# Kernel tuning notes

Hardware: AMD Instinct MI355X
Metric: run time of the kernel (lower is better)

## Reference

```python
import jax, jax.numpy as jnp
import numpy as np

EMSIZE = 1024
NHEAD = 16
HEAD = EMSIZE // NHEAD


def setup_inputs() -> dict:
    key = jax.random.key(0)
    ks = jax.random.split(key, 8)
    s = 1.0 / np.sqrt(EMSIZE)
    return {
        "embed": jax.random.normal(ks[0], (2, 2048, EMSIZE), dtype=jnp.float32),
        "q": jax.random.normal(ks[1], (2, 2048, EMSIZE), dtype=jnp.float32),
        "Wk": jax.random.normal(ks[2], (EMSIZE, EMSIZE), dtype=jnp.float32) * s,
        "bk": jnp.zeros((EMSIZE,), dtype=jnp.float32),
        "Wq": jax.random.normal(ks[3], (EMSIZE, EMSIZE), dtype=jnp.float32) * s,
        "bq": jnp.zeros((EMSIZE,), dtype=jnp.float32),
        "Wv": jax.random.normal(ks[4], (EMSIZE, EMSIZE), dtype=jnp.float32) * s,
        "bv": jnp.zeros((EMSIZE,), dtype=jnp.float32),
    }


def _split_heads(x):
    # [b, s, E] -> [b, h, s, d]
    b, s, _ = x.shape
    return x.reshape(b, s, NHEAD, HEAD).transpose(0, 2, 1, 3)


def reference(embed, q, Wk, bk, Wq, bq, Wv, bv):
    # torch Linear: y = x @ W.T + b
    k = _split_heads(embed @ Wk.T + bk)   # [b, h, skv, d]
    qh = _split_heads(q @ Wq.T + bq)      # [b, h, sq, d]
    v = _split_heads(embed @ Wv.T + bv)   # [b, h, skv, d]
    scale = 1.0 / np.sqrt(HEAD).astype(np.float32)
    scores = jnp.einsum("bhqd,bhkd->bhqk", qh, k) * scale
    attn = jax.nn.softmax(scores, axis=-1)  # dropout p=0 -> identity
    ctx = jnp.einsum("bhqk,bhkd->bhqd", attn, v)
    b, h, sq, d = ctx.shape
    return ctx.transpose(0, 2, 1, 3).reshape(b, sq, h * d)
```

## Files before the change

kernel.cpp:

```cpp
#include <hip/hip_runtime.h>
#include <cstdint>
#include <cstddef>


using bf16 = __bf16;
typedef __bf16 bf16x8 __attribute__((ext_vector_type(8)));
typedef float f32x4 __attribute__((ext_vector_type(4)));
typedef float f32x16 __attribute__((ext_vector_type(16)));
using uint32 = unsigned int;

__device__ __forceinline__ void async16(void* lds, const void* g) {
  __builtin_amdgcn_global_load_lds((__attribute__((address_space(1))) void*)g,
                                   (__attribute__((address_space(3))) void*)lds,
                                   16, 0, 0);
}

__device__ __forceinline__ uint32 pack_bf16x2(float lo, float hi_) {
  union { bf16 h[2]; uint32 u; } w;
  w.h[0] = (bf16)lo; w.h[1] = (bf16)hi_;
  return w.u;
}

__global__ void cast_all_kernel(const float* __restrict__ e, const float* __restrict__ q,
                                const float* __restrict__ wk, const float* __restrict__ wq,
                                const float* __restrict__ wv, bf16* __restrict__ dst) {
  int i = blockIdx.x * blockDim.x + threadIdx.x;
  if (i >= 2883584) return;
  const float* src; int off;
  if (i < 1048576)      { src = e;  off = 0; }
  else if (i < 2097152) { src = q;  off = 1048576; }
  else if (i < 2359296) { src = wk; off = 2097152; }
  else if (i < 2621440) { src = wq; off = 2359296; }
  else                  { src = wv; off = 2621440; }
  float4 v = reinterpret_cast<const float4*>(src)[i - off];
  union { bf16 h[4]; unsigned long long u; } o;
  o.h[0] = (bf16)v.x; o.h[1] = (bf16)v.y; o.h[2] = (bf16)v.z; o.h[3] = (bf16)v.w;
  reinterpret_cast<unsigned long long*>(dst)[i] = o.u;
}

__global__ __launch_bounds__(256) void proj_kernel(
    const bf16* __restrict__ emb, const bf16* __restrict__ qin,
    const bf16* __restrict__ wk, const bf16* __restrict__ wq, const bf16* __restrict__ wv,
    const float* __restrict__ bk, const float* __restrict__ bq, const float* __restrict__ bv,
    bf16* __restrict__ Kp, bf16* __restrict__ Qp, bf16* __restrict__ Vt)
{
  __shared__ bf16 As[128 * 64];
  __shared__ bf16 Bs[128 * 64];

  int pid = blockIdx.x;
  int proj = pid >> 8;
  int t = pid & 255;
  int m0 = (t >> 3) * 128;
  int n0 = (t & 7) * 128;

  const bf16* A = (proj == 1) ? qin : emb;
  const bf16* W = (proj == 0) ? wk : (proj == 1) ? wq : wv;
  const float* bias = (proj == 0) ? bk : (proj == 1) ? bq : bv;
  const bool proj2 = (proj == 2);

  int tid = threadIdx.x;
  int lane = tid & 63, wid = tid >> 6;
  int quad = lane >> 4, l16 = lane & 15;
  int moff = (wid & 1) * 64, noff = (wid >> 1) * 64;

  f32x4 zero = {0.f, 0.f, 0.f, 0.f};
  f32x4 acc[4][4];
#pragma unroll
  for (int i = 0; i < 4; i++)
#pragma unroll
    for (int j = 0; j < 4; j++) acc[i][j] = zero;

  for (int kk = 0; kk < 1024; kk += 64) {
    __syncthreads();
#pragma unroll
    for (int i = 0; i < 4; i++) {
      int c = i * 256 + tid;
      int row = c >> 3;
      int ko = ((c ^ row) & 7) << 3;
      async16(&As[(size_t)(i * 256 + wid * 64) * 8], &A[(size_t)(m0 + row) * 1024 + kk + ko]);
      async16(&Bs[(size_t)(i * 256 + wid * 64) * 8], &W[(size_t)(n0 + row) * 1024 + kk + ko]);
    }
    __syncthreads();
#pragma unroll
    for (int ks = 0; ks < 2; ks++) {
      bf16x8 af[4], bfr[4];
#pragma unroll
      for (int i = 0; i < 4; i++) {
        int row = moff + i * 16 + l16;
        af[i] = *reinterpret_cast<const bf16x8*>(&As[row * 64 + ((((ks << 2) | quad) ^ row) & 7) * 8]);
      }
#pragma unroll
      for (int j = 0; j < 4; j++) {
        int row = noff + j * 16 + l16;
        bfr[j] = *reinterpret_cast<const bf16x8*>(&Bs[row * 64 + ((((ks << 2) | quad) ^ row) & 7) * 8]);
      }
      if (proj2) {
#pragma unroll
        for (int i = 0; i < 4; i++)
#pragma unroll
          for (int j = 0; j < 4; j++)
            acc[i][j] = __builtin_amdgcn_mfma_f32_16x16x32_bf16(bfr[j], af[i], acc[i][j], 0, 0, 0);
      } else {
#pragma unroll
        for (int i = 0; i < 4; i++)
#pragma unroll
          for (int j = 0; j < 4; j++)
            acc[i][j] = __builtin_amdgcn_mfma_f32_16x16x32_bf16(af[i], bfr[j], acc[i][j], 0, 0, 0);
      }
    }
  }

  if (proj2) {
#pragma unroll
    for (int i = 0; i < 4; i++) {
      int grow = m0 + moff + i * 16 + l16;
      int bb = grow >> 11;
      int ss = grow & 2047;
#pragma unroll
      for (int j = 0; j < 4; j++) {
#pragma unroll
        for (int r = 0; r < 4; r++) {
          int gcol = n0 + noff + j * 16 + quad * 4 + r;
          int hh = gcol >> 6, dd = gcol & 63;
          int bh = bb * 16 + hh;
          float v = acc[i][j][r] + bias[gcol];
          Vt[((size_t)bh * 64 + dd) * 2048 + ss] = (bf16)v;
        }
      }
    }
  } else {
    float bvv[4];
#pragma unroll
    for (int j = 0; j < 4; j++) bvv[j] = bias[n0 + noff + j * 16 + l16];
    bf16* dst = (proj == 0) ? Kp : Qp;
    const float qs = (proj == 1) ? 0.18033688011112042f : 1.0f;
#pragma unroll
    for (int i = 0; i < 4; i++) {
#pragma unroll
      for (int r = 0; r < 4; r++) {
        int grow = m0 + moff + i * 16 + quad * 4 + r;
        int bb = grow >> 11;
        int ss = grow & 2047;
#pragma unroll
        for (int j = 0; j < 4; j++) {
          int gcol = n0 + noff + j * 16 + l16;
          int hh = gcol >> 6, dd = gcol & 63;
          int bh = bb * 16 + hh;
          float v = (acc[i][j][r] + bvv[j]) * qs;
          dst[((size_t)bh * 2048 + ss) * 64 + dd] = (bf16)v;
        }
      }
    }
  }
}

__global__ __launch_bounds__(256, 2) void attn_kernel(
    const bf16* __restrict__ Qp, const bf16* __restrict__ Kp, const bf16* __restrict__ Vt,
    float* __restrict__ out)
{
  __shared__ bf16 Ks[2][64 * 64];
  __shared__ bf16 Vs[2][64 * 64];

  int swz = (blockIdx.x & 7) * 64 + (blockIdx.x >> 3);
  int qblk = swz & 15;
  int bh = swz >> 4;
  int q0 = qblk << 7;
  int bb = bh >> 4, hh = bh & 15;

  const bf16* Qg = Qp + (size_t)bh * (2048 * 64);
  const bf16* Kg = Kp + (size_t)bh * (2048 * 64);
  const bf16* Vg = Vt + (size_t)bh * (64 * 2048);

  int tid = threadIdx.x, lane = tid & 63, wid = tid >> 6;
  int l32 = lane & 31;
  int h = lane >> 5;
  int wq0 = q0 + wid * 32;

  auto stage = [&](int kt_, int buf) {
#pragma unroll
    for (int i = 0; i < 2; i++) {
      int c = i * 256 + tid;
      int row = c >> 3;
      int srow = (row & ~12) | ((row & 4) << 1) | ((row & 8) >> 1);
      int ko = ((c ^ row) & 7) << 3;
      async16(&Ks[buf][(size_t)(i * 256 + wid * 64) * 8], &Kg[(size_t)(kt_ * 64 + srow) * 64 + ko]);
      async16(&Vs[buf][(size_t)(i * 256 + wid * 64) * 8], &Vg[(size_t)row * 2048 + kt_ * 64 + ko]);
    }
  };

  bf16x8 qf[4];
#pragma unroll
  for (int s = 0; s < 4; s++)
    qf[s] = *reinterpret_cast<const bf16x8*>(
        &Qg[(size_t)(wq0 + l32) * 64 + s * 16 + h * 8]);

  stage(0, 0);

  const f32x16 z16 = {0.f, 0.f, 0.f, 0.f, 0.f, 0.f, 0.f, 0.f,
                      0.f, 0.f, 0.f, 0.f, 0.f, 0.f, 0.f, 0.f};
  f32x16 Ov[2];
  Ov[0] = z16; Ov[1] = z16;
  float2 l2;
  l2.x = 0.f; l2.y = 0.f;

  for (int kt = 0; kt < 32; kt++) {
    int cur = kt & 1;
    __syncthreads();
    __builtin_amdgcn_sched_barrier(0);
    if (kt < 31) stage(kt + 1, cur ^ 1);
    __builtin_amdgcn_sched_barrier(0);

    const bf16* Kc = Ks[cur];
    const bf16* Vc = Vs[cur];

#pragma unroll
    for (int t = 0; t < 2; t++) {
      f32x16 St;
      int row = t * 32 + l32;
      {
        bf16x8 kf = *reinterpret_cast<const bf16x8*>(&Kc[row * 64 + ((h ^ row) & 7) * 8]);
        St = __builtin_amdgcn_mfma_f32_32x32x16_bf16(kf, qf[0], z16, 0, 0, 0);
      }
#pragma unroll
      for (int s = 1; s < 4; s++) {
        int j8 = s * 2 + h;
        bf16x8 kf = *reinterpret_cast<const bf16x8*>(&Kc[row * 64 + ((j8 ^ row) & 7) * 8]);
        St = __builtin_amdgcn_mfma_f32_32x32x16_bf16(kf, qf[s], St, 0, 0, 0);
      }

      uint32 pk[8];
#pragma unroll
      for (int i = 0; i < 8; i++) {
        float pe = __builtin_amdgcn_exp2f(St[2 * i]);
        float po = __builtin_amdgcn_exp2f(St[2 * i + 1]);
        l2.x += pe; l2.y += po;
        pk[i] = pack_bf16x2(pe, po);
      }

#pragma unroll
      for (int g = 0; g < 2; g++) {
        union { uint32 u[4]; bf16x8 v; } pb;
#pragma unroll
        for (int i = 0; i < 4; i++) pb.u[i] = pk[g * 4 + i];
        int j8 = t * 4 + g * 2 + h;
#pragma unroll
        for (int dt = 0; dt < 2; dt++) {
          int rowv = dt * 32 + l32;
          bf16x8 vf = *reinterpret_cast<const bf16x8*>(&Vc[rowv * 64 + ((j8 ^ rowv) & 7) * 8]);
          Ov[dt] = __builtin_amdgcn_mfma_f32_32x32x16_bf16(vf, pb.v, Ov[dt], 0, 0, 0);
        }
      }
    }
  }

  {
    float l_half = l2.x + l2.y;
    float l_tot = l_half + __shfl_xor(l_half, 32);
    float inv = 1.0f / l_tot;
    int q = wq0 + l32;
    float* dstO = out + ((size_t)bb * 2048 + q) * 1024 + hh * 64;
#pragma unroll
    for (int dt = 0; dt < 2; dt++)
#pragma unroll
      for (int g = 0; g < 4; g++) {
        float4 o;
        o.x = Ov[dt][4 * g + 0] * inv;
        o.y = Ov[dt][4 * g + 1] * inv;
        o.z = Ov[dt][4 * g + 2] * inv;
        o.w = Ov[dt][4 * g + 3] * inv;
        *reinterpret_cast<float4*>(&dstO[dt * 32 + g * 8 + 4 * h]) = o;
      }
  }
}

extern "C" void kernel_launch(void* const* d_in, const int* in_sizes, int n_in,
                              void* d_out, int out_size, void* d_ws, size_t ws_size,
                              hipStream_t stream) {
  (void)in_sizes; (void)n_in; (void)out_size; (void)ws_size;
  const float* embed = (const float*)d_in[0];
  const float* qin   = (const float*)d_in[1];
  const float* Wk    = (const float*)d_in[2];
  const float* bk    = (const float*)d_in[3];
  const float* Wq    = (const float*)d_in[4];
  const float* bq    = (const float*)d_in[5];
  const float* Wv    = (const float*)d_in[6];
  const float* bv    = (const float*)d_in[7];
  float* out = (float*)d_out;

  bf16* ws = (bf16*)d_ws;
  bf16* emb_bf = ws;
  bf16* q_bf   = emb_bf + 4194304;
  bf16* wk_bf  = q_bf   + 4194304;
  bf16* wq_bf  = wk_bf  + 1048576;
  bf16* wv_bf  = wq_bf  + 1048576;
  bf16* Kp     = wv_bf  + 1048576;
  bf16* Qp     = Kp     + 4194304;
  bf16* Vt     = Qp     + 4194304;

  cast_all_kernel<<<11264, 256, 0, stream>>>(embed, qin, Wk, Wq, Wv, ws);

  proj_kernel<<<768, 256, 0, stream>>>(emb_bf, q_bf, wk_bf, wq_bf, wv_bf,
                                       bk, bq, bv, Kp, Qp, Vt);
  attn_kernel<<<512, 256, 0, stream>>>(Qp, Kp, Vt, out);
}
```

Baseline: 187.2 us.

## Split attention key tiles across two wave groups and reduce partial outputs in LDS

The attention block grows from 256 to 512 threads. Each group of four waves now handles one 32-key half of every 64-key tile instead of one wave looping over both halves. At the end the second group writes its partial O accumulators and row sums into the reused K/V LDS buffers, and the first group adds them in before normalizing and storing. The aim is more waves in flight per CU to hide MFMA and exp latency, at the cost of an extra LDS reduction, an extra barrier, and a higher launch-bounds occupancy target that may limit registers.

```diff
diff --git a/kernel.cpp b/kernel.cpp
--- a/kernel.cpp
+++ b/kernel.cpp
@@ -154,12 +154,13 @@
   }
 }
 
-__global__ __launch_bounds__(256, 2) void attn_kernel(
+__global__ __launch_bounds__(512, 4) void attn_kernel(
     const bf16* __restrict__ Qp, const bf16* __restrict__ Kp, const bf16* __restrict__ Vt,
     float* __restrict__ out)
 {
   __shared__ bf16 Ks[2][64 * 64];
   __shared__ bf16 Vs[2][64 * 64];
+  __shared__ float lshare[256];
 
   int swz = (blockIdx.x & 7) * 64 + (blockIdx.x >> 3);
   int qblk = swz & 15;
@@ -174,18 +175,17 @@
   int tid = threadIdx.x, lane = tid & 63, wid = tid >> 6;
   int l32 = lane & 31;
   int h = lane >> 5;
-  int wq0 = q0 + wid * 32;
+  int qw = wid & 3;
+  int t = wid >> 2;
+  int wq0 = q0 + qw * 32;
 
   auto stage = [&](int kt_, int buf) {
-#pragma unroll
-    for (int i = 0; i < 2; i++) {
-      int c = i * 256 + tid;
-      int row = c >> 3;
-      int srow = (row & ~12) | ((row & 4) << 1) | ((row & 8) >> 1);
-      int ko = ((c ^ row) & 7) << 3;
-      async16(&Ks[buf][(size_t)(i * 256 + wid * 64) * 8], &Kg[(size_t)(kt_ * 64 + srow) * 64 + ko]);
-      async16(&Vs[buf][(size_t)(i * 256 + wid * 64) * 8], &Vg[(size_t)row * 2048 + kt_ * 64 + ko]);
-    }
+    int c = tid;
+    int row = c >> 3;
+    int srow = (row & ~12) | ((row & 4) << 1) | ((row & 8) >> 1);
+    int ko = ((c ^ row) & 7) << 3;
+    async16(&Ks[buf][(size_t)(wid * 64) * 8], &Kg[(size_t)(kt_ * 64 + srow) * 64 + ko]);
+    async16(&Vs[buf][(size_t)(wid * 64) * 8], &Vg[(size_t)row * 2048 + kt_ * 64 + ko]);
   };
 
   bf16x8 qf[4];
@@ -203,6 +203,8 @@
   float2 l2;
   l2.x = 0.f; l2.y = 0.f;
 
+  int row = t * 32 + l32;
+
   for (int kt = 0; kt < 32; kt++) {
     int cur = kt & 1;
     __syncthreads();
@@ -213,49 +215,74 @@
     const bf16* Kc = Ks[cur];
     const bf16* Vc = Vs[cur];
 
-#pragma unroll
-    for (int t = 0; t < 2; t++) {
-      f32x16 St;
-      int row = t * 32 + l32;
-      {
-        bf16x8 kf = *reinterpret_cast<const bf16x8*>(&Kc[row * 64 + ((h ^ row) & 7) * 8]);
-        St = __builtin_amdgcn_mfma_f32_32x32x16_bf16(kf, qf[0], z16, 0, 0, 0);
-      }
-#pragma unroll
-      for (int s = 1; s < 4; s++) {
-        int j8 = s * 2 + h;
-        bf16x8 kf = *reinterpret_cast<const bf16x8*>(&Kc[row * 64 + ((j8 ^ row) & 7) * 8]);
-        St = __builtin_amdgcn_mfma_f32_32x32x16_bf16(kf, qf[s], St, 0, 0, 0);
-      }
-
-      uint32 pk[8];
-#pragma unroll
-      for (int i = 0; i < 8; i++) {
-        float pe = __builtin_amdgcn_exp2f(St[2 * i]);
-        float po = __builtin_amdgcn_exp2f(St[2 * i + 1]);
-        l2.x += pe; l2.y += po;
-        pk[i] = pack_bf16x2(pe, po);
-      }
-
-#pragma unroll
-      for (int g = 0; g < 2; g++) {
-        union { uint32 u[4]; bf16x8 v; } pb;
-#pragma unroll
-        for (int i = 0; i < 4; i++) pb.u[i] = pk[g * 4 + i];
-        int j8 = t * 4 + g * 2 + h;
-#pragma unroll
-        for (int dt = 0; dt < 2; dt++) {
-          int rowv = dt * 32 + l32;
-          bf16x8 vf = *reinterpret_cast<const bf16x8*>(&Vc[rowv * 64 + ((j8 ^ rowv) & 7) * 8]);
-          Ov[dt] = __builtin_amdgcn_mfma_f32_32x32x16_bf16(vf, pb.v, Ov[dt], 0, 0, 0);
-        }
-      }
-    }
-  }
-
-  {
-    float l_half = l2.x + l2.y;
-    float l_tot = l_half + __shfl_xor(l_half, 32);
+    f32x16 St;
+    {
+      bf16x8 kf = *reinterpret_cast<const bf16x8*>(&Kc[row * 64 + ((h ^ row) & 7) * 8]);
+      St = __builtin_amdgcn_mfma_f32_32x32x16_bf16(kf, qf[0], z16, 0, 0, 0);
+    }
+#pragma unroll
+    for (int s = 1; s < 4; s++) {
+      int j8 = s * 2 + h;
+      bf16x8 kf = *reinterpret_cast<const bf16x8*>(&Kc[row * 64 + ((j8 ^ row) & 7) * 8]);
+      St = __builtin_amdgcn_mfma_f32_32x32x16_bf16(kf, qf[s], St, 0, 0, 0);
+    }
+
+    uint32 pk[8];
+#pragma unroll
+    for (int i = 0; i < 8; i++) {
+      float pe = __builtin_amdgcn_exp2f(St[2 * i]);
+      float po = __builtin_amdgcn_exp2f(St[2 * i + 1]);
+      l2.x += pe; l2.y += po;
+      pk[i] = pack_bf16x2(pe, po);
+    }
+
+#pragma unroll
+    for (int g = 0; g < 2; g++) {
+      union { uint32 u[4]; bf16x8 v; } pb;
+#pragma unroll
+      for (int i = 0; i < 4; i++) pb.u[i] = pk[g * 4 + i];
+      int j8 = t * 4 + g * 2 + h;
+#pragma unroll
+      for (int dt = 0; dt < 2; dt++) {
+        int rowv = dt * 32 + l32;
+        bf16x8 vf = *reinterpret_cast<const bf16x8*>(&Vc[rowv * 64 + ((j8 ^ rowv) & 7) * 8]);
+        Ov[dt] = __builtin_amdgcn_mfma_f32_32x32x16_bf16(vf, pb.v, Ov[dt], 0, 0, 0);
+      }
+    }
+  }
+
+  __syncthreads();
+  float* c0 = reinterpret_cast<float*>(&Ks[0][0]);
+  float* c1 = reinterpret_cast<float*>(&Vs[0][0]);
+  float lh = l2.x + l2.y;
+  if (t == 1) {
+#pragma unroll
+    for (int g = 0; g < 4; g++) {
+      int ci = (g * 256 + qw * 64 + lane) * 4;
+      float4 a, b;
+      a.x = Ov[0][4 * g + 0]; a.y = Ov[0][4 * g + 1];
+      a.z = Ov[0][4 * g + 2]; a.w = Ov[0][4 * g + 3];
+      b.x = Ov[1][4 * g + 0]; b.y = Ov[1][4 * g + 1];
+      b.z = Ov[1][4 * g + 2]; b.w = Ov[1][4 * g + 3];
+      *reinterpret_cast<float4*>(&c0[ci]) = a;
+      *reinterpret_cast<float4*>(&c1[ci]) = b;
+    }
+    lshare[qw * 64 + lane] = lh;
+  }
+  __syncthreads();
+  if (t == 0) {
+#pragma unroll
+    for (int g = 0; g < 4; g++) {
+      int ci = (g * 256 + qw * 64 + lane) * 4;
+      float4 a = *reinterpret_cast<const float4*>(&c0[ci]);
+      float4 b = *reinterpret_cast<const float4*>(&c1[ci]);
+      Ov[0][4 * g + 0] += a.x; Ov[0][4 * g + 1] += a.y;
+      Ov[0][4 * g + 2] += a.z; Ov[0][4 * g + 3] += a.w;
+      Ov[1][4 * g + 0] += b.x; Ov[1][4 * g + 1] += b.y;
+      Ov[1][4 * g + 2] += b.z; Ov[1][4 * g + 3] += b.w;
+    }
+    lh += lshare[qw * 64 + lane];
+    float l_tot = lh + __shfl_xor(lh, 32);
     float inv = 1.0f / l_tot;
     int q = wq0 + l32;
     float* dstO = out + ((size_t)bb * 2048 + q) * 1024 + hh * 64;
@@ -301,5 +328,5 @@
 
   proj_kernel<<<768, 256, 0, stream>>>(emb_bf, q_bf, wk_bf, wq_bf, wv_bf,
                                        bk, bq, bv, Kp, Qp, Vt);
-  attn_kernel<<<512, 256, 0, stream>>>(Qp, Kp, Vt, out);
-}
+  attn_kernel<<<512, 512, 0, stream>>>(Qp, Kp, Vt, out);
+}
```

After: 184.7 us. Within noise of the previous version (-1.3%).
